# Kernel optimization log

Hardware: AMD Instinct MI355X
Metric: run time of the kernel (lower is better)

## Reference

```python
import jax, jax.numpy as jnp
import numpy as np

NUM_EMBEDDINGS = 1024
EMBEDDING_DIM = 256
E_LOSS_WEIGHT = 0.25
MU = 0.01
EPSILON = 1e-05
N_TOKENS = 65536


def setup_inputs() -> dict:
    key = jax.random.key(0)
    k1, k2, k3 = jax.random.split(key, 3)
    return {
        "inputs": jax.random.normal(k1, (N_TOKENS, EMBEDDING_DIM), dtype=jnp.float32),
        "embedding_weight": jax.random.normal(k2, (NUM_EMBEDDINGS, EMBEDDING_DIM), dtype=jnp.float32),
        "ema_w": jax.random.normal(k3, (NUM_EMBEDDINGS, EMBEDDING_DIM), dtype=jnp.float32),
        "ema_cluster_size": jnp.zeros((NUM_EMBEDDINGS,), dtype=jnp.float32),
    }


def reference(inputs, embedding_weight, ema_w, ema_cluster_size):
    N, D = inputs.shape
    K = embedding_weight.shape[0]

    # Squared L2 distances: [N, K]
    distances = (
        jnp.sum(inputs ** 2, axis=1, keepdims=True)
        + jnp.sum(embedding_weight ** 2, axis=1)
        - 2.0 * (inputs @ embedding_weight.T)
    )
    idx = jnp.argmin(distances, axis=1)              # [N]

    # Gather codebook entries (replaces one-hot @ weight)
    quantized_raw = embedding_weight[idx]            # [N, D]

    # Commitment loss (quantized detached)
    e_latent_loss = jnp.mean((jax.lax.stop_gradient(quantized_raw) - inputs) ** 2)
    loss = E_LOSS_WEIGHT * e_latent_loss

    # Per-code counts and scatter-sum of inputs (replaces one-hot matmuls)
    counts = jax.ops.segment_sum(jnp.ones((N,), inputs.dtype), idx, num_segments=K)  # [K]
    dw = jax.ops.segment_sum(inputs, idx, num_segments=K)                             # [K, D]

    # EMA updates (training branch)
    new_cluster = ema_cluster_size * (1.0 - MU) + MU * counts
    n = jnp.sum(new_cluster)
    new_cluster = (new_cluster + EPSILON) / (n + K * EPSILON) * n
    new_ema_w = ema_w * (1.0 - MU) + MU * dw
    new_embedding = new_ema_w / new_cluster[:, None]

    # Straight-through estimator
    quantized = inputs + jax.lax.stop_gradient(quantized_raw - inputs)

    avg_probs = counts / N
    perplexity = jnp.exp(-jnp.sum(avg_probs * jnp.log(avg_probs + 1e-10)))

    encoding_indices = idx.reshape(N, 1)
    return quantized, loss, encoding_indices, perplexity, new_cluster, new_ema_w, new_embedding
```

## Files before the change

### kernel.cpp

```cpp
#include <hip/hip_runtime.h>

typedef _Float16 half8 __attribute__((ext_vector_type(8)));
typedef _Float16 half4 __attribute__((ext_vector_type(4)));
typedef float f32x4 __attribute__((ext_vector_type(4)));

#define N_TOK 65536
#define DIM   256
#define KCODE 1024
#define MU_C  0.01f
#define EPS_C 1e-5f

#define O_Q    0
#define O_LOSS 16777216
#define O_IDX  16777217
#define O_PERP 16842753
#define O_NC   16842754
#define O_NEW  16843778
#define O_EMB  17105922

#define W_IDX   0
#define W_CNT   65536
#define W_CUR   66560
#define W_OFF   67584
#define W_CNTF  68608
#define W_NFLAG 69632
#define W_FLAG  69696
#define W_ORDER 135232
#define W_DW    200768
#define W_WSQ   462912
#define W_WH    463936
#define W_XSQ   595008
#define W_ELATA 660544
#define W_PACK  676928
#define W_HALF  808000

__device__ __forceinline__ int imin(int a, int b) { return a < b ? a : b; }
__device__ __forceinline__ int imax(int a, int b) { return a > b ? a : b; }

__global__ void k_convert(const float* __restrict__ W, const float* __restrict__ X,
                          _Float16* __restrict__ Wh, _Float16* __restrict__ XhO,
                          float* __restrict__ wsq, float* __restrict__ xsq,
                          unsigned* __restrict__ wsu) {
    int gid = blockIdx.x * 256 + threadIdx.x;
    if (gid < 4097) wsu[W_CNT + gid] = 0u;
    if (gid < 65536) {
        ((float4*)(wsu + W_DW))[gid] = make_float4(0.f, 0.f, 0.f, 0.f);
        ((unsigned long long*)(wsu + W_PACK))[gid] = ~0ull;
    }
    int row  = blockIdx.x * 4 + (threadIdx.x >> 6);
    int lane = threadIdx.x & 63;
    const float* src;
    _Float16*    dst;
    if (row < KCODE) { src = W + (size_t)row * 256;            dst = Wh  + (size_t)row * 256; }
    else             { src = X + (size_t)(row - KCODE) * 256;  dst = XhO + (size_t)(row - KCODE) * 256; }
    float4 v = *(const float4*)(src + lane * 4);
    half4 h;
    h[0] = (_Float16)v.x; h[1] = (_Float16)v.y; h[2] = (_Float16)v.z; h[3] = (_Float16)v.w;
    *(half4*)(dst + lane * 4) = h;
    float s = v.x * v.x + v.y * v.y + v.z * v.z + v.w * v.w;
#pragma unroll
    for (int off = 1; off < 64; off <<= 1) s += __shfl_xor(s, off);
    if (lane == 0) {
        if (row < KCODE) wsq[row] = s;
        else             xsq[row - KCODE] = s;
    }
}

__global__ __launch_bounds__(256, 2) void argmin_mfma(
    const _Float16* __restrict__ Xh, const _Float16* __restrict__ Wh,
    const float* __restrict__ wsq, unsigned long long* __restrict__ halfres)
{
    __shared__ _Float16 Bs[2][32 * 256];

    const int tid  = threadIdx.x;
    const int lane = tid & 63;
    const int w    = tid >> 6;
    const int l15  = lane & 15;
    const int lk   = lane >> 4;
    const int half  = blockIdx.x & 1;
    const int cbase = half * 512;
    const int t0    = (blockIdx.x >> 1) * 256;

    half8 a[4][8];
#pragma unroll
    for (int g2 = 0; g2 < 4; ++g2) {
        const _Float16* xr = Xh + (size_t)(t0 + w * 64 + g2 * 16 + l15) * 256 + lk * 8;
#pragma unroll
        for (int g = 0; g < 8; ++g)
            a[g2][g] = *(const half8*)(xr + g * 32);
    }

    int u1a[16], u2a[16];
#pragma unroll
    for (int i = 0; i < 16; ++i) { u1a[i] = 0x7FFFFFFF; u2a[i] = 0x7FFFFFFF; }

#define STAGE(cc, bb)                                                          \
    _Pragma("unroll")                                                          \
    for (int i = 0; i < 4; ++i) {                                              \
        int loff = (w * 4 + i) * 1024;                                         \
        int off  = loff + lane * 16;                                           \
        int row  = off >> 9;                                                   \
        int slot = (off >> 4) & 31;                                            \
        const _Float16* src = Wh + (size_t)(cbase + (cc) * 32 + row) * 256     \
                                 + ((slot ^ row) << 3);                        \
        __builtin_amdgcn_global_load_lds(                                      \
            (const __attribute__((address_space(1))) void*)src,                \
            (__attribute__((address_space(3))) void*)((char*)Bs[bb] + loff),   \
            16, 0, 0);                                                         \
    }

    STAGE(0, 0);

    for (int c = 0; c < 16; ++c) {
        const int cur = c & 1;
        if (c < 15) {
            STAGE(c + 1, cur ^ 1);
            asm volatile("s_waitcnt vmcnt(4)" ::: "memory");
        } else {
            asm volatile("s_waitcnt vmcnt(0)" ::: "memory");
        }
        __builtin_amdgcn_s_barrier();

        f32x4 acc[4][2];
#pragma unroll
        for (int g2 = 0; g2 < 4; ++g2) { acc[g2][0] = (f32x4)0.0f; acc[g2][1] = (f32x4)0.0f; }

        __builtin_amdgcn_s_setprio(1);
#pragma unroll
        for (int ks = 0; ks < 8; ++ks) {
            const int j = ks * 4 + lk;
            const char* base = (const char*)Bs[cur];
            half8 b0 = *(const half8*)(base + l15 * 512        + ((j ^ l15) << 4));
            half8 b1 = *(const half8*)(base + (16 + l15) * 512 + ((j ^ (16 + l15)) << 4));
#pragma unroll
            for (int g2 = 0; g2 < 4; ++g2) {
                acc[g2][0] = __builtin_amdgcn_mfma_f32_16x16x32_f16(
                    a[g2][ks], b0, acc[g2][0], 0, 0, 0);
                acc[g2][1] = __builtin_amdgcn_mfma_f32_16x16x32_f16(
                    a[g2][ks], b1, acc[g2][1], 0, 0, 0);
            }
        }
        __builtin_amdgcn_s_setprio(0);

#pragma unroll
        for (int nf = 0; nf < 2; ++nf) {
            int   code = cbase + c * 32 + nf * 16 + l15;
            float tc   = fmaf(0.5f, wsq[code], 512.0f);
#pragma unroll
            for (int g2 = 0; g2 < 4; ++g2)
#pragma unroll
                for (int r = 0; r < 4; ++r) {
                    float sv = tc - acc[g2][nf][r];
                    int u = (__float_as_int(sv) & 0xFFFFFC00) | code;
                    int s = g2 * 4 + r;
                    u2a[s] = imin(u2a[s], imax(u1a[s], u));
                    u1a[s] = imin(u1a[s], u);
                }
        }
        __builtin_amdgcn_s_barrier();
    }
#undef STAGE

#pragma unroll
    for (int s = 0; s < 16; ++s) {
#pragma unroll
        for (int off = 1; off < 16; off <<= 1) {
            int b1 = __shfl_xor(u1a[s], off);
            int b2 = __shfl_xor(u2a[s], off);
            int n2 = imin(imin(u2a[s], b2), imax(u1a[s], b1));
            u1a[s] = imin(u1a[s], b1);
            u2a[s] = n2;
        }
    }
    if (l15 == 0) {
#pragma unroll
        for (int s = 0; s < 16; ++s) {
            int row = t0 + w * 64 + (s >> 2) * 16 + lk * 4 + (s & 3);
            halfres[(size_t)half * 65536 + row] =
                ((unsigned long long)(unsigned)u1a[s] << 32) | (unsigned)u2a[s];
        }
    }
}

__global__ void merge_halves(const unsigned long long* __restrict__ halfres,
                             int* __restrict__ idx_out, float* __restrict__ out,
                             unsigned* __restrict__ cnt,
                             unsigned* __restrict__ nflag, int* __restrict__ flaglist)
{
    int t = blockIdx.x * 256 + threadIdx.x;
    unsigned long long A = halfres[t], B = halfres[65536 + t];
    int a1 = (int)(A >> 32), a2 = (int)(unsigned)A;
    int b1 = (int)(B >> 32), b2 = (int)(unsigned)B;
    int u1 = imin(a1, b1);
    int u2 = imin(imax(a1, b1), imin(a2, b2));
    int code = u1 & 1023;
    idx_out[t] = code;
    out[O_IDX + t] = (float)code;
    atomicAdd(&cnt[code], 1u);
    float s1 = __int_as_float(u1 & 0xFFFFFC00);
    float s2 = __int_as_float(u2 & 0xFFFFFC00);
    if (s2 - s1 < 0.125f) {
        unsigned p = atomicAdd(nflag, 1u);
        flaglist[p] = t;
    }
}

__global__ __launch_bounds__(256, 2) void cleanup_gemm(
    const float* __restrict__ X, const float* __restrict__ W,
    const float* __restrict__ wsq, const unsigned* __restrict__ nflagp,
    const int* __restrict__ flaglist, const float* __restrict__ xsq_all,
    unsigned long long* __restrict__ pack)
{
    __shared__ float xs [16][64];
    __shared__ float wps[16][128];
    __shared__ float wsq_s[128];

    const int n = (int)nflagp[0];
    const int tid = threadIdx.x;
    const int tx  = tid & 15;
    const int ty  = tid >> 4;
    const int c0    = (blockIdx.x & 7) * 128;
    const int tslot = blockIdx.x >> 3;
    const int srow_x = tid & 63,  sq_x = tid >> 6;
    const int srow_w = tid & 127, sh_w = tid >> 7;

    if (tid < 128) wsq_s[tid] = wsq[c0 + tid];

    for (int tile = tslot; tile * 64 < n; tile += 256) {
        const int t0 = tile * 64;
        const int gtok = flaglist[imin(t0 + srow_x, n - 1)];
        const float* xrow = X + (size_t)gtok * DIM;
        const float* wrow = W + (size_t)(c0 + srow_w) * DIM + sh_w * 8;

        float xsq_r[4];
#pragma unroll
        for (int i = 0; i < 4; ++i)
            xsq_r[i] = xsq_all[flaglist[imin(t0 + ty * 4 + i, n - 1)]];

        float minv[4]; int mini[4];
#pragma unroll
        for (int i = 0; i < 4; ++i) { minv[i] = 3.402823466e+38f; mini[i] = 0; }

        float acc[4][8];
#pragma unroll
        for (int i = 0; i < 4; ++i)
#pragma unroll
            for (int j = 0; j < 8; ++j) acc[i][j] = 0.0f;

        float4 xa = *(const float4*)(xrow + sq_x * 4);
        float4 wa = *(const float4*)(wrow);
        float4 wb = *(const float4*)(wrow + 4);

        for (int ks = 0; ks < 16; ++ks) {
            __syncthreads();
            xs[sq_x * 4 + 0][srow_x] = xa.x; xs[sq_x * 4 + 1][srow_x] = xa.y;
            xs[sq_x * 4 + 2][srow_x] = xa.z; xs[sq_x * 4 + 3][srow_x] = xa.w;
            wps[sh_w * 8 + 0][srow_w] = wa.x; wps[sh_w * 8 + 1][srow_w] = wa.y;
            wps[sh_w * 8 + 2][srow_w] = wa.z; wps[sh_w * 8 + 3][srow_w] = wa.w;
            wps[sh_w * 8 + 4][srow_w] = wb.x; wps[sh_w * 8 + 5][srow_w] = wb.y;
            wps[sh_w * 8 + 6][srow_w] = wb.z; wps[sh_w * 8 + 7][srow_w] = wb.w;
            __syncthreads();
            if (ks < 15) {
                xa = *(const float4*)(xrow + (ks + 1) * 16 + sq_x * 4);
                wa = *(const float4*)(wrow + (ks + 1) * 16);
                wb = *(const float4*)(wrow + (ks + 1) * 16 + 4);
            }
#pragma unroll
            for (int kl = 0; kl < 16; ++kl) {
                float4 av = *(const float4*)&xs [kl][ty * 4];
                float4 b0 = *(const float4*)&wps[kl][tx * 8];
                float4 b1 = *(const float4*)&wps[kl][tx * 8 + 4];
                float aa[4] = {av.x, av.y, av.z, av.w};
                float bb[8] = {b0.x, b0.y, b0.z, b0.w, b1.x, b1.y, b1.z, b1.w};
#pragma unroll
                for (int i = 0; i < 4; ++i)
#pragma unroll
                    for (int j = 0; j < 8; ++j)
                        acc[i][j] = fmaf(aa[i], bb[j], acc[i][j]);
            }
        }
#pragma unroll
        for (int i = 0; i < 4; ++i) {
#pragma unroll
            for (int j = 0; j < 8; ++j) {
                float t1 = xsq_r[i] + wsq_s[tx * 8 + j];
                float s  = t1 - 2.0f * acc[i][j];
                int   cc = c0 + tx * 8 + j;
                if (s < minv[i]) { minv[i] = s; mini[i] = cc; }
            }
        }
#pragma unroll
        for (int i = 0; i < 4; ++i) {
#pragma unroll
            for (int off = 1; off < 16; off <<= 1) {
                float ov = __shfl_xor(minv[i], off);
                int   oi = __shfl_xor(mini[i], off);
                if (ov < minv[i] || (ov == minv[i] && oi < mini[i])) {
                    minv[i] = ov; mini[i] = oi;
                }
            }
        }
        if (tx == 0) {
#pragma unroll
            for (int i = 0; i < 4; ++i) {
                int pos = t0 + ty * 4 + i;
                if (pos < n) {
                    unsigned long long pu =
                        ((unsigned long long)(unsigned)__float_as_int(minv[i]) << 32)
                        | (unsigned)mini[i];
                    atomicMin(&pack[pos], pu);
                }
            }
        }
        __syncthreads();
    }
}

__global__ void cleanup_write(const unsigned* __restrict__ nflagp,
                              const int* __restrict__ flaglist,
                              const unsigned long long* __restrict__ pack,
                              int* __restrict__ idx_out, float* __restrict__ out,
                              unsigned* __restrict__ cnt) {
    int n = (int)nflagp[0];
    for (int i = blockIdx.x * 256 + threadIdx.x; i < n; i += 65536) {
        int t = flaglist[i];
        int code = (int)(pack[i] & 0xFFFFFFFFull);
        int old  = idx_out[t];
        if (code != old) {
            idx_out[t] = code;
            out[O_IDX + t] = (float)code;
            atomicAdd(&cnt[code], 1u);
            atomicAdd(&cnt[old], 0xFFFFFFFFu);
        }
    }
}

__global__ __launch_bounds__(256) void k_scan(const unsigned* __restrict__ cnt,
                                              unsigned* __restrict__ offs,
                                              float* __restrict__ cntf) {
    int t = threadIdx.x, lane = t & 63, wid = t >> 6;
    uint4 v = ((const uint4*)cnt)[t];
    cntf[4 * t + 0] = (float)v.x; cntf[4 * t + 1] = (float)v.y;
    cntf[4 * t + 2] = (float)v.z; cntf[4 * t + 3] = (float)v.w;
    unsigned s = v.x + v.y + v.z + v.w;
    unsigned ps = s;
#pragma unroll
    for (int off = 1; off < 64; off <<= 1) {
        unsigned o = __shfl_up(ps, off);
        if (lane >= off) ps += o;
    }
    __shared__ unsigned wsum[4];
    if (lane == 63) wsum[wid] = ps;
    __syncthreads();
    unsigned base = 0;
#pragma unroll
    for (int i = 0; i < 4; ++i) if (i < wid) base += wsum[i];
    unsigned excl = base + ps - s;
    offs[4 * t + 0] = excl;
    offs[4 * t + 1] = excl + v.x;
    offs[4 * t + 2] = excl + v.x + v.y;
    offs[4 * t + 3] = excl + v.x + v.y + v.z;
}

__global__ void k_scatter(const int* __restrict__ idx, const unsigned* __restrict__ offs,
                          unsigned* __restrict__ cursor, unsigned* __restrict__ order) {
    int t = blockIdx.x * 256 + threadIdx.x;
    int c = idx[t];
    unsigned p = atomicAdd(&cursor[c], 1u);
    order[offs[c] + p] = ((unsigned)c << 16) | (unsigned)t;
}

__global__ __launch_bounds__(256) void k_epilogue_dw(
    const float* __restrict__ X, const float* __restrict__ W,
    const unsigned* __restrict__ order, float* __restrict__ out,
    float* __restrict__ dw, float* __restrict__ elat_arr)
{
    int gw   = (blockIdx.x * 256 + threadIdx.x) >> 6;
    int lane = threadIdx.x & 63;
    int p0 = gw * 16;
    float4 acc = make_float4(0.f, 0.f, 0.f, 0.f);
    float4 wreg = make_float4(0.f, 0.f, 0.f, 0.f);
    int cur = -1;
    float e = 0.f;
#pragma unroll 4
    for (int i = 0; i < 16; ++i) {
        unsigned u = order[p0 + i];
        int t = (int)(u & 0xFFFFu), c = (int)(u >> 16);
        float4 x4 = *(const float4*)(X + (size_t)t * 256 + lane * 4);
        if (c != cur) {
            if (cur >= 0) {
                float* dwp = dw + (size_t)cur * 256 + lane * 4;
                atomicAdd(dwp + 0, acc.x); atomicAdd(dwp + 1, acc.y);
                atomicAdd(dwp + 2, acc.z); atomicAdd(dwp + 3, acc.w);
            }
            wreg = *(const float4*)(W + (size_t)c * 256 + lane * 4);
            cur = c; acc = x4;
        } else {
            acc.x += x4.x; acc.y += x4.y; acc.z += x4.z; acc.w += x4.w;
        }
        ((float4*)(out + O_Q))[(size_t)t * 64 + lane] = wreg;
        float d0 = wreg.x - x4.x, d1 = wreg.y - x4.y;
        float d2 = wreg.z - x4.z, d3 = wreg.w - x4.w;
        e += d0 * d0 + d1 * d1 + d2 * d2 + d3 * d3;
    }
    if (cur >= 0) {
        float* dwp = dw + (size_t)cur * 256 + lane * 4;
        atomicAdd(dwp + 0, acc.x); atomicAdd(dwp + 1, acc.y);
        atomicAdd(dwp + 2, acc.z); atomicAdd(dwp + 3, acc.w);
    }
#pragma unroll
    for (int off = 1; off < 64; off <<= 1) e += __shfl_xor(e, off);
    __shared__ float se[4];
    int wid = threadIdx.x >> 6;
    if (lane == 0) se[wid] = e;
    __syncthreads();
    if (threadIdx.x == 0) elat_arr[blockIdx.x] = se[0] + se[1] + se[2] + se[3];
}

__global__ __launch_bounds__(1024) void finalize_small(
    const float* __restrict__ ecs, const float* __restrict__ counts,
    const float* __restrict__ elat_arr, float* __restrict__ out)
{
    int k = threadIdx.x;
    float cnt = counts[k];
    float nc = ecs[k] * (1.0f - MU_C) + MU_C * cnt;
    float p = cnt * (1.0f / 65536.0f);
    float h = p * logf(p + 1e-10f);
    float el = elat_arr[k];
    float rn = nc, rh = h, re = el;
#pragma unroll
    for (int off = 1; off < 64; off <<= 1) {
        rn += __shfl_xor(rn, off);
        rh += __shfl_xor(rh, off);
        re += __shfl_xor(re, off);
    }
    __shared__ float sn[16], sh[16], sef[16];
    int wid = k >> 6, lane = k & 63;
    if (lane == 0) { sn[wid] = rn; sh[wid] = rh; sef[wid] = re; }
    __syncthreads();
    float n = 0.0f, H = 0.0f, E = 0.0f;
#pragma unroll
    for (int i = 0; i < 16; ++i) { n += sn[i]; H += sh[i]; E += sef[i]; }
    out[O_NC + k] = (nc + EPS_C) / (n + 1024.0f * EPS_C) * n;
    if (k == 0) {
        out[O_LOSS] = 0.25f * (E * (1.0f / 16777216.0f));
        out[O_PERP] = expf(-H);
    }
}

__global__ void finalize_embed(const float* __restrict__ ema_w,
                               const float* __restrict__ dw, float* __restrict__ out)
{
    int gid = blockIdx.x * blockDim.x + threadIdx.x;
    int k = gid >> 8;
    float ew = ema_w[gid] * (1.0f - MU_C) + MU_C * dw[gid];
    out[O_NEW + gid] = ew;
    out[O_EMB + gid] = ew / out[O_NC + k];
}

extern "C" void kernel_launch(void* const* d_in, const int* in_sizes, int n_in,
                              void* d_out, int out_size, void* d_ws, size_t ws_size,
                              hipStream_t stream) {
    const float* X     = (const float*)d_in[0];
    const float* W     = (const float*)d_in[1];
    const float* ema_w = (const float*)d_in[2];
    const float* ecs   = (const float*)d_in[3];
    float*    out    = (float*)d_out;
    unsigned* wsu    = (unsigned*)d_ws;
    float*    wsf    = (float*)d_ws;
    int*      idx    = (int*)d_ws + W_IDX;
    unsigned* cnt    = wsu + W_CNT;
    unsigned* cursor = wsu + W_CUR;
    unsigned* offs   = wsu + W_OFF;
    float*    cntf   = wsf + W_CNTF;
    unsigned* nflag  = wsu + W_NFLAG;
    int*      flags  = (int*)d_ws + W_FLAG;
    unsigned* order  = wsu + W_ORDER;
    float*    dw     = wsf + W_DW;
    float*    wsq    = wsf + W_WSQ;
    _Float16* Wh     = (_Float16*)(wsu + W_WH);
    float*    xsq    = wsf + W_XSQ;
    float*    elatA  = wsf + W_ELATA;
    unsigned long long* pack    = (unsigned long long*)(wsu + W_PACK);
    unsigned long long* halfres = (unsigned long long*)(wsu + W_HALF);
    _Float16* XhO    = (_Float16*)(out + O_Q);

    hipLaunchKernelGGL(k_convert,      dim3(16640), dim3(256),  0, stream, W, X, Wh, XhO, wsq, xsq, wsu);
    hipLaunchKernelGGL(argmin_mfma,    dim3(512),   dim3(256),  0, stream, XhO, Wh, wsq, halfres);
    hipLaunchKernelGGL(merge_halves,   dim3(256),   dim3(256),  0, stream, halfres, idx, out, cnt, nflag, flags);
    hipLaunchKernelGGL(cleanup_gemm,   dim3(2048),  dim3(256),  0, stream, X, W, wsq, nflag, flags, xsq, pack);
    hipLaunchKernelGGL(cleanup_write,  dim3(256),   dim3(256),  0, stream, nflag, flags, pack, idx, out, cnt);
    hipLaunchKernelGGL(k_scan,         dim3(1),     dim3(256),  0, stream, cnt, offs, cntf);
    hipLaunchKernelGGL(k_scatter,      dim3(256),   dim3(256),  0, stream, idx, offs, cursor, order);
    hipLaunchKernelGGL(k_epilogue_dw,  dim3(1024),  dim3(256),  0, stream, X, W, order, out, dw, elatA);
    hipLaunchKernelGGL(finalize_small, dim3(1),     dim3(1024), 0, stream, ecs, cntf, elatA, out);
    hipLaunchKernelGGL(finalize_embed, dim3(1024),  dim3(256),  0, stream, ema_w, dw, out);
}
```

Measured before the change: 211.7 us.

## Move quantized output and commitment loss into the merge kernel

Result: slower. 225.1 us (+6.3%).

```diff
diff --git a/kernel.cpp b/kernel.cpp
--- a/kernel.cpp
+++ b/kernel.cpp
@@ -182,27 +182,44 @@
     }
 }
 
-__global__ void merge_halves(const unsigned long long* __restrict__ halfres,
-                             int* __restrict__ idx_out, float* __restrict__ out,
-                             unsigned* __restrict__ cnt,
-                             unsigned* __restrict__ nflag, int* __restrict__ flaglist)
+__global__ __launch_bounds__(256) void merge_q(
+    const unsigned long long* __restrict__ halfres,
+    const float* __restrict__ X, const float* __restrict__ W,
+    int* __restrict__ idx_out, float* __restrict__ out,
+    unsigned* __restrict__ cnt, unsigned* __restrict__ nflag,
+    int* __restrict__ flaglist, float* __restrict__ elat_arr)
 {
-    int t = blockIdx.x * 256 + threadIdx.x;
+    int gid = blockIdx.x * 256 + threadIdx.x;
+    int t = gid >> 6, q = gid & 63;
     unsigned long long A = halfres[t], B = halfres[65536 + t];
     int a1 = (int)(A >> 32), a2 = (int)(unsigned)A;
     int b1 = (int)(B >> 32), b2 = (int)(unsigned)B;
     int u1 = imin(a1, b1);
     int u2 = imin(imax(a1, b1), imin(a2, b2));
     int code = u1 & 1023;
-    idx_out[t] = code;
-    out[O_IDX + t] = (float)code;
-    atomicAdd(&cnt[code], 1u);
-    float s1 = __int_as_float(u1 & 0xFFFFFC00);
-    float s2 = __int_as_float(u2 & 0xFFFFFC00);
-    if (s2 - s1 < 0.125f) {
-        unsigned p = atomicAdd(nflag, 1u);
-        flaglist[p] = t;
-    }
+    float4 x4 = ((const float4*)X)[gid];
+    float4 w4 = *(const float4*)(W + (size_t)code * 256 + q * 4);
+    ((float4*)(out + O_Q))[gid] = w4;
+    float d0 = w4.x - x4.x, d1 = w4.y - x4.y, d2 = w4.z - x4.z, d3 = w4.w - x4.w;
+    float e = d0 * d0 + d1 * d1 + d2 * d2 + d3 * d3;
+    if (q == 0) {
+        idx_out[t] = code;
+        out[O_IDX + t] = (float)code;
+        atomicAdd(&cnt[code], 1u);
+        float s1 = __int_as_float(u1 & 0xFFFFFC00);
+        float s2 = __int_as_float(u2 & 0xFFFFFC00);
+        if (s2 - s1 < 0.125f) {
+            unsigned p = atomicAdd(nflag, 1u);
+            flaglist[p] = t;
+        }
+    }
+#pragma unroll
+    for (int off = 1; off < 64; off <<= 1) e += __shfl_xor(e, off);
+    __shared__ float se[4];
+    int lane = threadIdx.x & 63, wid = threadIdx.x >> 6;
+    if (lane == 0) se[wid] = e;
+    __syncthreads();
+    if (threadIdx.x == 0) elat_arr[blockIdx.x] = se[0] + se[1] + se[2] + se[3];
 }
 
 __global__ __launch_bounds__(256, 2) void cleanup_gemm(
@@ -319,18 +336,34 @@
 __global__ void cleanup_write(const unsigned* __restrict__ nflagp,
                               const int* __restrict__ flaglist,
                               const unsigned long long* __restrict__ pack,
+                              const float* __restrict__ X, const float* __restrict__ W,
                               int* __restrict__ idx_out, float* __restrict__ out,
-                              unsigned* __restrict__ cnt) {
+                              unsigned* __restrict__ cnt, float* __restrict__ elat_arr) {
     int n = (int)nflagp[0];
-    for (int i = blockIdx.x * 256 + threadIdx.x; i < n; i += 65536) {
+    int wv   = (blockIdx.x * 256 + threadIdx.x) >> 6;
+    int lane = threadIdx.x & 63;
+    for (int i = wv; i < n; i += 1024) {
         int t = flaglist[i];
         int code = (int)(pack[i] & 0xFFFFFFFFull);
         int old  = idx_out[t];
         if (code != old) {
-            idx_out[t] = code;
-            out[O_IDX + t] = (float)code;
-            atomicAdd(&cnt[code], 1u);
-            atomicAdd(&cnt[old], 0xFFFFFFFFu);
+            float4 x4 = *(const float4*)(X + (size_t)t * 256 + lane * 4);
+            float4 wn = *(const float4*)(W + (size_t)code * 256 + lane * 4);
+            float4 wo = *(const float4*)(W + (size_t)old * 256 + lane * 4);
+            ((float4*)(out + O_Q))[(size_t)t * 64 + lane] = wn;
+            float n0 = wn.x - x4.x, n1 = wn.y - x4.y, n2 = wn.z - x4.z, n3 = wn.w - x4.w;
+            float o0 = wo.x - x4.x, o1 = wo.y - x4.y, o2 = wo.z - x4.z, o3 = wo.w - x4.w;
+            float de = (n0 * n0 + n1 * n1 + n2 * n2 + n3 * n3)
+                     - (o0 * o0 + o1 * o1 + o2 * o2 + o3 * o3);
+#pragma unroll
+            for (int off = 1; off < 64; off <<= 1) de += __shfl_xor(de, off);
+            if (lane == 0) {
+                idx_out[t] = code;
+                out[O_IDX + t] = (float)code;
+                atomicAdd(&cnt[code], 1u);
+                atomicAdd(&cnt[old], 0xFFFFFFFFu);
+                atomicAdd(&elat_arr[0], de);
+            }
         }
     }
 }
@@ -370,18 +403,15 @@
     order[offs[c] + p] = ((unsigned)c << 16) | (unsigned)t;
 }
 
-__global__ __launch_bounds__(256) void k_epilogue_dw(
-    const float* __restrict__ X, const float* __restrict__ W,
-    const unsigned* __restrict__ order, float* __restrict__ out,
-    float* __restrict__ dw, float* __restrict__ elat_arr)
+__global__ __launch_bounds__(256) void k_dw(
+    const float* __restrict__ X, const unsigned* __restrict__ order,
+    float* __restrict__ dw)
 {
     int gw   = (blockIdx.x * 256 + threadIdx.x) >> 6;
     int lane = threadIdx.x & 63;
     int p0 = gw * 16;
     float4 acc = make_float4(0.f, 0.f, 0.f, 0.f);
-    float4 wreg = make_float4(0.f, 0.f, 0.f, 0.f);
     int cur = -1;
-    float e = 0.f;
 #pragma unroll 4
     for (int i = 0; i < 16; ++i) {
         unsigned u = order[p0 + i];
@@ -393,28 +423,16 @@
                 atomicAdd(dwp + 0, acc.x); atomicAdd(dwp + 1, acc.y);
                 atomicAdd(dwp + 2, acc.z); atomicAdd(dwp + 3, acc.w);
             }
-            wreg = *(const float4*)(W + (size_t)c * 256 + lane * 4);
             cur = c; acc = x4;
         } else {
             acc.x += x4.x; acc.y += x4.y; acc.z += x4.z; acc.w += x4.w;
         }
-        ((float4*)(out + O_Q))[(size_t)t * 64 + lane] = wreg;
-        float d0 = wreg.x - x4.x, d1 = wreg.y - x4.y;
-        float d2 = wreg.z - x4.z, d3 = wreg.w - x4.w;
-        e += d0 * d0 + d1 * d1 + d2 * d2 + d3 * d3;
     }
     if (cur >= 0) {
         float* dwp = dw + (size_t)cur * 256 + lane * 4;
         atomicAdd(dwp + 0, acc.x); atomicAdd(dwp + 1, acc.y);
         atomicAdd(dwp + 2, acc.z); atomicAdd(dwp + 3, acc.w);
     }
-#pragma unroll
-    for (int off = 1; off < 64; off <<= 1) e += __shfl_xor(e, off);
-    __shared__ float se[4];
-    int wid = threadIdx.x >> 6;
-    if (lane == 0) se[wid] = e;
-    __syncthreads();
-    if (threadIdx.x == 0) elat_arr[blockIdx.x] = se[0] + se[1] + se[2] + se[3];
 }
 
 __global__ __launch_bounds__(1024) void finalize_small(
@@ -426,7 +444,9 @@
     float nc = ecs[k] * (1.0f - MU_C) + MU_C * cnt;
     float p = cnt * (1.0f / 65536.0f);
     float h = p * logf(p + 1e-10f);
-    float el = elat_arr[k];
+    float el = 0.f;
+#pragma unroll
+    for (int i = 0; i < 16; ++i) el += elat_arr[k + i * 1024];
     float rn = nc, rh = h, re = el;
 #pragma unroll
     for (int off = 1; off < 64; off <<= 1) {
@@ -487,12 +507,12 @@
 
     hipLaunchKernelGGL(k_convert,      dim3(16640), dim3(256),  0, stream, W, X, Wh, XhO, wsq, xsq, wsu);
     hipLaunchKernelGGL(argmin_mfma,    dim3(512),   dim3(256),  0, stream, XhO, Wh, wsq, halfres);
-    hipLaunchKernelGGL(merge_halves,   dim3(256),   dim3(256),  0, stream, halfres, idx, out, cnt, nflag, flags);
+    hipLaunchKernelGGL(merge_q,        dim3(16384), dim3(256),  0, stream, halfres, X, W, idx, out, cnt, nflag, flags, elatA);
     hipLaunchKernelGGL(cleanup_gemm,   dim3(2048),  dim3(256),  0, stream, X, W, wsq, nflag, flags, xsq, pack);
-    hipLaunchKernelGGL(cleanup_write,  dim3(256),   dim3(256),  0, stream, nflag, flags, pack, idx, out, cnt);
+    hipLaunchKernelGGL(cleanup_write,  dim3(256),   dim3(256),  0, stream, nflag, flags, pack, X, W, idx, out, cnt, elatA);
     hipLaunchKernelGGL(k_scan,         dim3(1),     dim3(256),  0, stream, cnt, offs, cntf);
     hipLaunchKernelGGL(k_scatter,      dim3(256),   dim3(256),  0, stream, idx, offs, cursor, order);
-    hipLaunchKernelGGL(k_epilogue_dw,  dim3(1024),  dim3(256),  0, stream, X, W, order, out, dw, elatA);
+    hipLaunchKernelGGL(k_dw,           dim3(1024),  dim3(256),  0, stream, X, order, dw);
     hipLaunchKernelGGL(finalize_small, dim3(1),     dim3(1024), 0, stream, ecs, cntf, elatA, out);
     hipLaunchKernelGGL(finalize_embed, dim3(1024),  dim3(256),  0, stream, ema_w, dw, out);
 }
```
